# Kernel tuning notes

Measured on AMD Instinct MI355X. Metric: run time of the kernel, lower is better.

Reference implementation:

```python
import jax, jax.numpy as jnp
import numpy as np

D = 1024
H = 16
FFN = 4096
B = 4
S = 1024
EPS = 1e-12
NEG = -1e9


def _layernorm(x, gamma, beta):
    mean = x.mean(-1, keepdims=True)
    var = ((x - mean) ** 2).mean(-1, keepdims=True)  # biased var, matches unbiased=False
    return gamma * (x - mean) * jax.lax.rsqrt(var + EPS) + beta


def setup_inputs() -> dict:
    key = jax.random.key(0)
    ks = jax.random.split(key, 16)
    s_in = 1.0 / np.sqrt(D)
    s_ff = 1.0 / np.sqrt(FFN)
    return {
        "x": jax.random.normal(ks[0], (B, S, D), dtype=jnp.float32),
        "mask": jax.random.randint(ks[1], (B, H, S), 0, 2) > 0,  # bernoulli(0.5) key mask
        "Wqkv": jax.random.uniform(ks[2], (3 * D, D), minval=-s_in, maxval=s_in),
        "bqkv": jax.random.uniform(ks[3], (3 * D,), minval=-s_in, maxval=s_in),
        "Wo": jax.random.uniform(ks[4], (D, D), minval=-s_in, maxval=s_in),
        "bo": jax.random.uniform(ks[5], (D,), minval=-s_in, maxval=s_in),
        "W1": jax.random.uniform(ks[6], (FFN, D), minval=-s_in, maxval=s_in),
        "b1": jax.random.uniform(ks[7], (FFN,), minval=-s_in, maxval=s_in),
        "W2": jax.random.uniform(ks[8], (D, FFN), minval=-s_ff, maxval=s_ff),
        "b2": jax.random.uniform(ks[9], (D,), minval=-s_ff, maxval=s_ff),
        "g1": jnp.ones((D,), jnp.float32),
        "be1": jnp.zeros((D,), jnp.float32),
        "g2": jnp.ones((D,), jnp.float32),
        "be2": jnp.zeros((D,), jnp.float32),
    }


def reference(x, mask, Wqkv, bqkv, Wo, bo, W1, b1, W2, b2, g1, be1, g2, be2):
    b, s, _ = x.shape
    hd = D // H
    scale = hd ** -0.5

    # --- ProbSparseSelfAttention (dropout in eval mode) ---
    qkv = x @ Wqkv.T + bqkv                                   # [b, s, 3D]
    q, k, v = jnp.split(qkv, 3, axis=-1)
    q = q.reshape(b, s, H, hd).transpose(0, 2, 1, 3)          # [b, h, s, d]
    k = k.reshape(b, s, H, hd).transpose(0, 2, 1, 3)
    v = v.reshape(b, s, H, hd).transpose(0, 2, 1, 3)
    scores = jnp.einsum('bhid,bhjd->bhij', q * scale, k)      # [b, h, s, s]
    scores = jnp.where(mask[:, :, None, :], scores, NEG)      # mask keys (broadcast over i)
    attn = jax.nn.softmax(scores, axis=-1)
    ctx = jnp.einsum('bhij,bhjd->bhid', attn, v)
    ctx = ctx.transpose(0, 2, 1, 3).reshape(b, s, D)
    attn_out = ctx @ Wo.T + bo

    # residual + LayerNorm 1
    h = _layernorm(attn_out + x, g1, be1)

    # --- FFN ---
    ff = jax.nn.relu(h @ W1.T + b1) @ W2.T + b2

    # residual + LayerNorm 2
    return _layernorm(ff + h, g2, be2)
```

## Files before the change

kernel.cpp:

```cpp
#include <hip/hip_runtime.h>

#define DDIM 1024
#define FFN_DIM 4096
#define SS 1024
#define MTOK 4096

typedef __bf16 bf16x8 __attribute__((ext_vector_type(8)));
typedef float f32x4 __attribute__((ext_vector_type(4)));
typedef unsigned short ushort4v __attribute__((ext_vector_type(4)));
typedef unsigned short ushort8v __attribute__((ext_vector_type(8)));

__device__ __forceinline__ unsigned short f2bf(float f) {
    union { float f; unsigned u; } x;
    x.f = f;
    unsigned r = x.u + 0x7FFFu + ((x.u >> 16) & 1u);
    return (unsigned short)(r >> 16);
}
__device__ __forceinline__ float bf2f(unsigned short u) {
    union { unsigned u; float f; } x;
    x.u = (unsigned)u << 16;
    return x.f;
}

__device__ __forceinline__ int swz(int off) {
    return off ^ ((((off >> 7) & 7) ^ ((off >> 10) & 1)) << 4);
}
__device__ __forceinline__ int gswz(int b) {
    return b ^ (((b >> 7) & 7) << 4);
}

__device__ __forceinline__ void gload_lds16(const void* g, void* l) {
    __builtin_amdgcn_global_load_lds(
        (__attribute__((address_space(1))) unsigned int*)(unsigned long long)(g),
        (__attribute__((address_space(3))) unsigned int*)(l), 16, 0, 0);
}

__global__ __launch_bounds__(256) void cvt_bf16(const float* __restrict__ in,
                                                unsigned short* __restrict__ out, int n4) {
    int i = blockIdx.x * 256 + threadIdx.x;
    if (i < n4) {
        float4 v = ((const float4*)in)[i];
        ushort4v u = {f2bf(v.x), f2bf(v.y), f2bf(v.z), f2bf(v.w)};
        ((ushort4v*)out)[i] = u;
    }
}

template <int EPI, int SPLITK>
__global__ __launch_bounds__(512, 2) void gemm256(const unsigned short* __restrict__ A,
                                                  const unsigned short* __restrict__ B,
                                                  const float* __restrict__ bias,
                                                  unsigned short* __restrict__ O0,
                                                  unsigned short* __restrict__ O1,
                                                  unsigned short* __restrict__ O2,
                                                  unsigned short* __restrict__ O3,
                                                  int M, int N, int K) {
    __shared__ char smem[131072];
    const int tid = threadIdx.x;
    const int wid = tid >> 6, lane = tid & 63;
    const int wm = wid >> 2, wn = wid & 3;
    const int lr = lane & 15, lkb = (lane >> 4) * 16;
    const int m0 = blockIdx.y * 256, n0 = blockIdx.x * 256;
    const int z = blockIdx.z;
    const int Kc = K / SPLITK, kb = z * Kc;
    const int NT = Kc / 64;

    f32x4 acc[8][4];
#pragma unroll
    for (int i = 0; i < 8; i++)
#pragma unroll
        for (int j = 0; j < 4; j++) acc[i][j] = (f32x4){0.f, 0.f, 0.f, 0.f};

    auto stage_half = [&](int c, int t, int hs) {
        const int op = hs >> 1, h = hs & 1;
        const unsigned short* G = op ? B : A;
        const int r0 = (op ? n0 : m0) + h * 128;
        char* base = smem + c * 65536 + op * 32768 + h * 16384;
        const int k0 = kb + t * 64;
#pragma unroll
        for (int q = 0; q < 2; q++) {
            int d = q * 8192 + wid * 1024 + lane * 16;
            int s = gswz(d);
            int row = s >> 7, colb = s & 127;
            gload_lds16(G + (size_t)(r0 + row) * K + k0 + (colb >> 1),
                        base + q * 8192 + wid * 1024);
        }
    };

    stage_half(0, 0, 0); stage_half(0, 0, 1); stage_half(0, 0, 2); stage_half(0, 0, 3);
    asm volatile("s_waitcnt vmcnt(0)" ::: "memory");
    __syncthreads();

    for (int t = 0; t < NT; ++t) {
        const int c = t & 1;
        const char* Ab = smem + c * 65536;
        const char* Bb = Ab + 32768;
        const bool pre = (t + 1 < NT);
        bf16x8 bfr[4][2];
#pragma unroll
        for (int p = 0; p < 4; ++p) {
            bf16x8 afr[2][2];
#pragma unroll
            for (int mi = 0; mi < 2; mi++)
#pragma unroll
                for (int ks = 0; ks < 2; ks++) {
                    int b = (wm * 128 + (p * 2 + mi) * 16 + lr) * 128 + ks * 64 + lkb;
                    afr[mi][ks] = *(const bf16x8*)(Ab + gswz(b));
                }
            if (p == 0) {
#pragma unroll
                for (int nb = 0; nb < 4; nb++)
#pragma unroll
                    for (int ks = 0; ks < 2; ks++) {
                        int b = (wn * 64 + nb * 16 + lr) * 128 + ks * 64 + lkb;
                        bfr[nb][ks] = *(const bf16x8*)(Bb + gswz(b));
                    }
            }
            if (pre) stage_half(c ^ 1, t + 1, p);
            __builtin_amdgcn_s_barrier();
            asm volatile("s_waitcnt lgkmcnt(0)" ::: "memory");
            __builtin_amdgcn_sched_barrier(0);
            __builtin_amdgcn_s_setprio(1);
#pragma unroll
            for (int mi = 0; mi < 2; mi++)
#pragma unroll
                for (int nb = 0; nb < 4; nb++)
#pragma unroll
                    for (int ks = 0; ks < 2; ks++)
                        acc[p * 2 + mi][nb] = __builtin_amdgcn_mfma_f32_16x16x32_bf16(
                            afr[mi][ks], bfr[nb][ks], acc[p * 2 + mi][nb], 0, 0, 0);
            __builtin_amdgcn_s_setprio(0);
            if (p == 3 && pre) asm volatile("s_waitcnt vmcnt(0)" ::: "memory");
            __builtin_amdgcn_s_barrier();
        }
    }

    unsigned short* Op = (SPLITK == 1) ? O0 : (z == 0 ? O0 : z == 1 ? O1 : z == 2 ? O2 : O3);
    float bv[4];
#pragma unroll
    for (int nb = 0; nb < 4; nb++) bv[nb] = (z == 0) ? bias[n0 + wn * 64 + nb * 16 + lr] : 0.f;
    const int rr = (lane >> 4) * 4;
#pragma unroll
    for (int mb = 0; mb < 8; mb++)
#pragma unroll
        for (int nb = 0; nb < 4; nb++) {
            int col = n0 + wn * 64 + nb * 16 + lr;
#pragma unroll
            for (int r = 0; r < 4; r++) {
                int row = m0 + wm * 128 + mb * 16 + rr + r;
                float v = acc[mb][nb][r] + bv[nb];
                if (EPI == 2) v = fmaxf(v, 0.f);
                Op[(size_t)row * N + col] = f2bf(v);
            }
        }
}

__global__ __launch_bounds__(256) void gemm_bt(const unsigned short* __restrict__ A,
                                               const unsigned short* __restrict__ B,
                                               const float* __restrict__ bias,
                                               unsigned short* __restrict__ Cout,
                                               int M, int N, int K) {
    __shared__ unsigned short Asm[2][128 * 32];
    __shared__ unsigned short Bsm[2][128 * 32];
    const int tid = threadIdx.x;
    const int wid = tid >> 6, lane = tid & 63;
    const int m0 = blockIdx.y * 128, n0 = blockIdx.x * 128;
    const int lr = lane & 15, lk = (lane >> 4) * 8;
    const int wr = (wid >> 1) * 64, wc = (wid & 1) * 64;
    const int nkt = K / 32;

    f32x4 acc[4][4];
#pragma unroll
    for (int i = 0; i < 4; i++)
#pragma unroll
        for (int j = 0; j < 4; j++) acc[i][j] = (f32x4){0.f, 0.f, 0.f, 0.f};

    const unsigned short* Ag = A + (size_t)m0 * K;
    const unsigned short* Bg = B + (size_t)n0 * K;

    auto stage = [&](int buf, int k0) {
#pragma unroll
        for (int p = 0; p < 2; ++p) {
            int idx = p * 4096 + wid * 1024 + lane * 16;
            int row = idx >> 6, ce = (idx & 63) >> 1;
            gload_lds16(Ag + (size_t)row * K + k0 + ce, (char*)Asm[buf] + p * 4096 + wid * 1024);
            gload_lds16(Bg + (size_t)row * K + k0 + ce, (char*)Bsm[buf] + p * 4096 + wid * 1024);
        }
    };

    stage(0, 0);
    for (int kt = 0; kt < nkt; ++kt) {
        const int cur = kt & 1;
        __syncthreads();
        if (kt + 1 < nkt) stage(cur ^ 1, (kt + 1) * 32);
        bf16x8 af[4], bfr[4];
#pragma unroll
        for (int m = 0; m < 4; m++) af[m] = *(const bf16x8*)&Asm[cur][(wr + m * 16 + lr) * 32 + lk];
#pragma unroll
        for (int n = 0; n < 4; n++) bfr[n] = *(const bf16x8*)&Bsm[cur][(wc + n * 16 + lr) * 32 + lk];
#pragma unroll
        for (int m = 0; m < 4; m++)
#pragma unroll
            for (int n = 0; n < 4; n++)
                acc[m][n] = __builtin_amdgcn_mfma_f32_16x16x32_bf16(af[m], bfr[n], acc[m][n], 0, 0, 0);
    }

    float bv[4];
#pragma unroll
    for (int n = 0; n < 4; n++) bv[n] = bias[n0 + wc + n * 16 + lr];
    const int r0 = (lane >> 4) * 4;
#pragma unroll
    for (int m = 0; m < 4; m++)
#pragma unroll
        for (int n = 0; n < 4; n++) {
            int col = n0 + wc + n * 16 + lr;
#pragma unroll
            for (int r = 0; r < 4; r++) {
                int row = m0 + wr + m * 16 + r0 + r;
                Cout[(size_t)row * N + col] = f2bf(acc[m][n][r] + bv[n]);
            }
        }
}

__global__ __launch_bounds__(256) void vtrans(const unsigned short* __restrict__ qkv,
                                              unsigned short* __restrict__ vt) {
    __shared__ unsigned short T[64 * 64];
    const int tid = threadIdx.x;
    const int bh = blockIdx.y, b = bh >> 4, h = bh & 15;
    const int s0 = blockIdx.x * 64;
    const unsigned short* src = qkv + (size_t)(b * SS + s0) * 3072 + 2048 + h * 64;
#pragma unroll
    for (int p = 0; p < 2; p++) {
        int idx = p * 4096 + tid * 16;
        int row = idx >> 7, ce = (idx & 127) >> 1;
        ushort8v v = *(const ushort8v*)(src + (size_t)row * 3072 + ce);
        *(ushort8v*)((char*)T + swz(idx)) = v;
    }
    __syncthreads();
    unsigned short* dst = vt + (size_t)bh * 64 * SS + s0;
#pragma unroll
    for (int p = 0; p < 2; p++) {
        int idx = p * 4096 + tid * 16;
        int d = idx >> 7, t0 = (idx & 127) >> 1;
        ushort8v o;
#pragma unroll
        for (int i = 0; i < 8; i++)
            o[i] = *(const unsigned short*)((char*)T + swz((t0 + i) * 128 + d * 2));
        *(ushort8v*)(dst + (size_t)d * SS + t0) = o;
    }
}

__global__ __launch_bounds__(256) void attn_fused(const unsigned short* __restrict__ qkv,
                                                  const unsigned short* __restrict__ vt,
                                                  const int* __restrict__ mask,
                                                  unsigned short* __restrict__ ctx) {
    __shared__ unsigned short Ksm[2][64 * 64];
    __shared__ unsigned short Vsm[2][64 * 64];
    __shared__ unsigned short Psm[4][16 * 64];
    __shared__ float maskadd[2][64];
    const int tid = threadIdx.x, wid = tid >> 6, lane = tid & 63;
    const int bid = blockIdx.x;
    const int xcd = bid & 7, loc = bid >> 3;
    const int bh = xcd * 8 + (loc >> 4), q0 = (loc & 15) * 64;
    const int b = bh >> 4, h = bh & 15;
    const int lr = lane & 15, lk2 = (lane >> 4) * 16;
    const size_t base = (size_t)b * SS * 3072 + h * 64;
    const float SC2 = 0.18033688011112042f;

    bf16x8 qf[2];
    {
        const unsigned short* qp = qkv + base + (size_t)(q0 + wid * 16 + lr) * 3072;
        qf[0] = *(const bf16x8*)(qp + (lk2 >> 1));
        qf[1] = *(const bf16x8*)(qp + 32 + (lk2 >> 1));
    }
    float m_run[4] = {-3e38f, -3e38f, -3e38f, -3e38f};
    float l_run[4] = {0.f, 0.f, 0.f, 0.f};
    f32x4 oacc[4];
#pragma unroll
    for (int i = 0; i < 4; i++) oacc[i] = (f32x4){0.f, 0.f, 0.f, 0.f};

    const unsigned short* Kgb = qkv + base + 1024;
    const unsigned short* Vgb = vt + (size_t)bh * 64 * SS;

    auto stage = [&](int buf, int kt) {
#pragma unroll
        for (int p = 0; p < 2; p++) {
            int idx = p * 4096 + wid * 1024 + lane * 16;
            int s = swz(idx);
            int row = s >> 7, ce = (s & 127) >> 1;
            gload_lds16(Kgb + (size_t)(kt * 64 + row) * 3072 + ce,
                        (char*)Ksm[buf] + p * 4096 + wid * 1024);
            gload_lds16(Vgb + (size_t)row * SS + kt * 64 + ce,
                        (char*)Vsm[buf] + p * 4096 + wid * 1024);
        }
        if (tid < 64) maskadd[buf][tid] = mask[bh * SS + kt * 64 + tid] ? 0.f : -1.5e9f;
    };

    stage(0, 0);
    for (int kt = 0; kt < SS / 64; ++kt) {
        const int cur = kt & 1;
        __syncthreads();
        if (kt < SS / 64 - 1) stage(cur ^ 1, kt + 1);
        const char* Kb = (const char*)Ksm[cur];
        const char* Vb = (const char*)Vsm[cur];

        f32x4 sc[4];
#pragma unroll
        for (int nt = 0; nt < 4; nt++) {
            f32x4 a = (f32x4){0.f, 0.f, 0.f, 0.f};
            int rowb = (nt * 16 + lr) * 128;
            bf16x8 k0v = *(const bf16x8*)(Kb + swz(rowb + lk2));
            bf16x8 k1v = *(const bf16x8*)(Kb + swz(rowb + 64 + lk2));
            a = __builtin_amdgcn_mfma_f32_16x16x32_bf16(qf[0], k0v, a, 0, 0, 0);
            a = __builtin_amdgcn_mfma_f32_16x16x32_bf16(qf[1], k1v, a, 0, 0, 0);
            sc[nt] = a;
        }
        float mk[4];
#pragma unroll
        for (int nt = 0; nt < 4; nt++) mk[nt] = maskadd[cur][nt * 16 + lr];
        float pmax[4];
#pragma unroll
        for (int r = 0; r < 4; r++) {
            float v = -3e38f;
#pragma unroll
            for (int nt = 0; nt < 4; nt++) {
                float s = sc[nt][r] * SC2 + mk[nt];
                sc[nt][r] = s;
                v = fmaxf(v, s);
            }
            v = fmaxf(v, __shfl_xor(v, 1));
            v = fmaxf(v, __shfl_xor(v, 2));
            v = fmaxf(v, __shfl_xor(v, 4));
            v = fmaxf(v, __shfl_xor(v, 8));
            pmax[r] = v;
        }
        bool okt = true;
#pragma unroll
        for (int r = 0; r < 4; r++) okt = okt && (pmax[r] <= m_run[r] + 8.f);
        const bool skip = __all(okt);
        if (!skip) {
#pragma unroll
            for (int r = 0; r < 4; r++) {
                float mnew = fmaxf(m_run[r], pmax[r]);
                float alpha = exp2f(m_run[r] - mnew);
                m_run[r] = mnew;
                l_run[r] *= alpha;
#pragma unroll
                for (int dt = 0; dt < 4; dt++) oacc[dt][r] *= alpha;
            }
        }
#pragma unroll
        for (int r = 0; r < 4; r++) {
            float ls = 0.f;
#pragma unroll
            for (int nt = 0; nt < 4; nt++) {
                float pexp = exp2f(sc[nt][r] - m_run[r]);
                sc[nt][r] = pexp;
                ls += pexp;
            }
            ls += __shfl_xor(ls, 1);
            ls += __shfl_xor(ls, 2);
            ls += __shfl_xor(ls, 4);
            ls += __shfl_xor(ls, 8);
            l_run[r] += ls;
        }
        const int prow = (lane >> 4) * 4;
        char* Pb = (char*)Psm[wid];
#pragma unroll
        for (int nt = 0; nt < 4; nt++)
#pragma unroll
            for (int r = 0; r < 4; r++)
                *(unsigned short*)(Pb + swz((prow + r) * 128 + (nt * 16 + lr) * 2)) = f2bf(sc[nt][r]);
        bf16x8 pf0 = *(const bf16x8*)(Pb + swz(lr * 128 + lk2));
        bf16x8 pf1 = *(const bf16x8*)(Pb + swz(lr * 128 + 64 + lk2));
#pragma unroll
        for (int dt = 0; dt < 4; dt++) {
            int rowb = (dt * 16 + lr) * 128;
            bf16x8 v0 = *(const bf16x8*)(Vb + swz(rowb + lk2));
            bf16x8 v1 = *(const bf16x8*)(Vb + swz(rowb + 64 + lk2));
            oacc[dt] = __builtin_amdgcn_mfma_f32_16x16x32_bf16(pf0, v0, oacc[dt], 0, 0, 0);
            oacc[dt] = __builtin_amdgcn_mfma_f32_16x16x32_bf16(pf1, v1, oacc[dt], 0, 0, 0);
        }
    }
#pragma unroll
    for (int dt = 0; dt < 4; dt++)
#pragma unroll
        for (int r = 0; r < 4; r++) {
            float v = oacc[dt][r] / l_run[r];
            int row = q0 + wid * 16 + (lane >> 4) * 4 + r;
            ctx[(size_t)(b * SS + row) * DDIM + h * 64 + dt * 16 + lr] = f2bf(v);
        }
}

__global__ __launch_bounds__(256) void resid_ln1(const unsigned short* __restrict__ attno,
                                                 const float* __restrict__ x,
                                                 const float* __restrict__ gamma,
                                                 const float* __restrict__ beta,
                                                 unsigned short* __restrict__ hbf) {
    __shared__ float red[16];
    const int row = blockIdx.x, tid = threadIdx.x;
    const int wid = tid >> 6, lane = tid & 63;
    ushort4v av = ((const ushort4v*)(attno + (size_t)row * DDIM))[tid];
    float4 bv = ((const float4*)(x + (size_t)row * DDIM))[tid];
    float4 v;
    v.x = bf2f(av[0]) + bv.x; v.y = bf2f(av[1]) + bv.y;
    v.z = bf2f(av[2]) + bv.z; v.w = bf2f(av[3]) + bv.w;
    float s = v.x + v.y + v.z + v.w;
    float s2 = v.x * v.x + v.y * v.y + v.z * v.z + v.w * v.w;
#pragma unroll
    for (int off = 1; off < 64; off <<= 1) { s += __shfl_xor(s, off); s2 += __shfl_xor(s2, off); }
    if (lane == 0) { red[wid] = s; red[8 + wid] = s2; }
    __syncthreads();
    s = red[0] + red[1] + red[2] + red[3];
    s2 = red[8] + red[9] + red[10] + red[11];
    float mean = s * (1.f / 1024.f);
    float var = s2 * (1.f / 1024.f) - mean * mean;
    float rstd = rsqrtf(var + 1e-12f);
    float4 g = ((const float4*)gamma)[tid];
    float4 be = ((const float4*)beta)[tid];
    ushort4v u = {f2bf(g.x * (v.x - mean) * rstd + be.x),
                  f2bf(g.y * (v.y - mean) * rstd + be.y),
                  f2bf(g.z * (v.z - mean) * rstd + be.z),
                  f2bf(g.w * (v.w - mean) * rstd + be.w)};
    ((ushort4v*)(hbf + (size_t)row * DDIM))[tid] = u;
}

__global__ __launch_bounds__(256) void resid_ln2(const unsigned short* __restrict__ p0,
                                                 const unsigned short* __restrict__ p1,
                                                 const unsigned short* __restrict__ p2,
                                                 const unsigned short* __restrict__ p3,
                                                 const unsigned short* __restrict__ hbf,
                                                 const float* __restrict__ gamma,
                                                 const float* __restrict__ beta,
                                                 float* __restrict__ out) {
    __shared__ float red[16];
    const int row = blockIdx.x, tid = threadIdx.x;
    const int wid = tid >> 6, lane = tid & 63;
    size_t off = (size_t)row * DDIM;
    ushort4v a0 = ((const ushort4v*)(p0 + off))[tid];
    ushort4v a1 = ((const ushort4v*)(p1 + off))[tid];
    ushort4v a2 = ((const ushort4v*)(p2 + off))[tid];
    ushort4v a3 = ((const ushort4v*)(p3 + off))[tid];
    ushort4v hv = ((const ushort4v*)(hbf + off))[tid];
    float4 v;
    v.x = bf2f(a0[0]) + bf2f(a1[0]) + bf2f(a2[0]) + bf2f(a3[0]) + bf2f(hv[0]);
    v.y = bf2f(a0[1]) + bf2f(a1[1]) + bf2f(a2[1]) + bf2f(a3[1]) + bf2f(hv[1]);
    v.z = bf2f(a0[2]) + bf2f(a1[2]) + bf2f(a2[2]) + bf2f(a3[2]) + bf2f(hv[2]);
    v.w = bf2f(a0[3]) + bf2f(a1[3]) + bf2f(a2[3]) + bf2f(a3[3]) + bf2f(hv[3]);
    float s = v.x + v.y + v.z + v.w;
    float s2 = v.x * v.x + v.y * v.y + v.z * v.z + v.w * v.w;
#pragma unroll
    for (int off2 = 1; off2 < 64; off2 <<= 1) { s += __shfl_xor(s, off2); s2 += __shfl_xor(s2, off2); }
    if (lane == 0) { red[wid] = s; red[8 + wid] = s2; }
    __syncthreads();
    s = red[0] + red[1] + red[2] + red[3];
    s2 = red[8] + red[9] + red[10] + red[11];
    float mean = s * (1.f / 1024.f);
    float var = s2 * (1.f / 1024.f) - mean * mean;
    float rstd = rsqrtf(var + 1e-12f);
    float4 g = ((const float4*)gamma)[tid];
    float4 be = ((const float4*)beta)[tid];
    float4 o;
    o.x = g.x * (v.x - mean) * rstd + be.x;
    o.y = g.y * (v.y - mean) * rstd + be.y;
    o.z = g.z * (v.z - mean) * rstd + be.z;
    o.w = g.w * (v.w - mean) * rstd + be.w;
    ((float4*)(out + off))[tid] = o;
}

extern "C" void kernel_launch(void* const* d_in, const int* in_sizes, int n_in,
                              void* d_out, int out_size, void* d_ws, size_t ws_size,
                              hipStream_t stream) {
    const float* x    = (const float*)d_in[0];
    const int*   mask = (const int*)d_in[1];
    const float* Wqkv = (const float*)d_in[2];
    const float* bqkv = (const float*)d_in[3];
    const float* Wo   = (const float*)d_in[4];
    const float* bo   = (const float*)d_in[5];
    const float* W1   = (const float*)d_in[6];
    const float* b1   = (const float*)d_in[7];
    const float* W2   = (const float*)d_in[8];
    const float* b2   = (const float*)d_in[9];
    const float* g1   = (const float*)d_in[10];
    const float* be1  = (const float*)d_in[11];
    const float* g2   = (const float*)d_in[12];
    const float* be2  = (const float*)d_in[13];
    float* out = (float*)d_out;

    char* ws = (char*)d_ws;
    unsigned short* xbf   = (unsigned short*)(ws + 0);
    unsigned short* vtb   = (unsigned short*)(ws + 0);
    unsigned short* p0    = (unsigned short*)(ws + 0);
    unsigned short* qkvbf = (unsigned short*)(ws + (8ull << 20));
    unsigned short* ff1   = (unsigned short*)(ws + (8ull << 20));
    unsigned short* ctx   = (unsigned short*)(ws + (32ull << 20));
    unsigned short* w1b   = (unsigned short*)(ws + (40ull << 20));
    unsigned short* p1    = (unsigned short*)(ws + (40ull << 20));
    unsigned short* w2b   = (unsigned short*)(ws + (48ull << 20));
    unsigned short* wqkvb = (unsigned short*)(ws + (56ull << 20));
    unsigned short* p2    = (unsigned short*)(ws + (56ull << 20));
    unsigned short* wob   = (unsigned short*)(ws + (62ull << 20));
    unsigned short* attno = (unsigned short*)(ws + (64ull << 20));
    unsigned short* p3    = (unsigned short*)(ws + (64ull << 20));
    unsigned short* hbf   = (unsigned short*)(ws + (72ull << 20));

    cvt_bf16<<<4096, 256, 0, stream>>>(x, xbf, 1048576);
    cvt_bf16<<<3072, 256, 0, stream>>>(Wqkv, wqkvb, 786432);
    cvt_bf16<<<1024, 256, 0, stream>>>(Wo, wob, 262144);
    cvt_bf16<<<4096, 256, 0, stream>>>(W1, w1b, 1048576);
    cvt_bf16<<<4096, 256, 0, stream>>>(W2, w2b, 1048576);

    gemm256<1, 1><<<dim3(12, 16, 1), 512, 0, stream>>>(xbf, wqkvb, bqkv,
        qkvbf, qkvbf, qkvbf, qkvbf, MTOK, 3072, 1024);
    vtrans<<<dim3(16, 64), 256, 0, stream>>>(qkvbf, vtb);
    attn_fused<<<1024, 256, 0, stream>>>(qkvbf, vtb, mask, ctx);
    gemm_bt<<<dim3(8, 32), 256, 0, stream>>>(ctx, wob, bo, attno, MTOK, 1024, 1024);
    resid_ln1<<<4096, 256, 0, stream>>>(attno, x, g1, be1, hbf);
    gemm256<2, 1><<<dim3(16, 16, 1), 512, 0, stream>>>(hbf, w1b, b1,
        ff1, ff1, ff1, ff1, MTOK, FFN_DIM, 1024);
    gemm256<1, 4><<<dim3(4, 16, 4), 512, 0, stream>>>(ff1, w2b, b2,
        p0, p1, p2, p3, MTOK, DDIM, FFN_DIM);
    resid_ln2<<<4096, 256, 0, stream>>>(p0, p1, p2, p3, hbf, g2, be2, out);
}
```

Measured before the change: 372.2 us.

## Merge fp32-to-bf16 conversions into one launch and issue full-tile prefetch at once

The five separate conversion kernels are replaced by a single kernel that picks source and destination by thread index, which removes four launches and their tail gaps. In the 256x256 GEMM, the next K-tile's global-to-LDS loads are now all issued in the first sub-step instead of being spread over four sub-steps. The float-to-bf16 helper now uses the compiler's native cast instead of manual rounding. Issuing all prefetch loads at once may raise VMEM pressure early and shift how well loads overlap with MFMA work.

```diff
diff --git a/kernel.cpp b/kernel.cpp
--- a/kernel.cpp
+++ b/kernel.cpp
@@ -11,10 +11,8 @@
 typedef unsigned short ushort8v __attribute__((ext_vector_type(8)));
 
 __device__ __forceinline__ unsigned short f2bf(float f) {
-    union { float f; unsigned u; } x;
-    x.f = f;
-    unsigned r = x.u + 0x7FFFu + ((x.u >> 16) & 1u);
-    return (unsigned short)(r >> 16);
+    __bf16 h = (__bf16)f;
+    return __builtin_bit_cast(unsigned short, h);
 }
 __device__ __forceinline__ float bf2f(unsigned short u) {
     union { unsigned u; float f; } x;
@@ -35,14 +33,28 @@
         (__attribute__((address_space(3))) unsigned int*)(l), 16, 0, 0);
 }
 
-__global__ __launch_bounds__(256) void cvt_bf16(const float* __restrict__ in,
-                                                unsigned short* __restrict__ out, int n4) {
+__global__ __launch_bounds__(256) void cvt_all(const float* __restrict__ x,
+                                               const float* __restrict__ wqkv,
+                                               const float* __restrict__ wo,
+                                               const float* __restrict__ w1,
+                                               const float* __restrict__ w2,
+                                               unsigned short* __restrict__ xbf,
+                                               unsigned short* __restrict__ wqkvb,
+                                               unsigned short* __restrict__ wob,
+                                               unsigned short* __restrict__ w1b,
+                                               unsigned short* __restrict__ w2b) {
     int i = blockIdx.x * 256 + threadIdx.x;
-    if (i < n4) {
-        float4 v = ((const float4*)in)[i];
-        ushort4v u = {f2bf(v.x), f2bf(v.y), f2bf(v.z), f2bf(v.w)};
-        ((ushort4v*)out)[i] = u;
-    }
+    const float* src;
+    unsigned short* dst;
+    int off;
+    if (i < 1048576)      { src = x;    dst = xbf;   off = i; }
+    else if (i < 1835008) { src = wqkv; dst = wqkvb; off = i - 1048576; }
+    else if (i < 2097152) { src = wo;   dst = wob;   off = i - 1835008; }
+    else if (i < 3145728) { src = w1;   dst = w1b;   off = i - 2097152; }
+    else                  { src = w2;   dst = w2b;   off = i - 3145728; }
+    float4 v = ((const float4*)src)[off];
+    ushort4v u = {f2bf(v.x), f2bf(v.y), f2bf(v.z), f2bf(v.w)};
+    ((ushort4v*)dst)[off] = u;
 }
 
 template <int EPI, int SPLITK>
@@ -70,23 +82,25 @@
 #pragma unroll
         for (int j = 0; j < 4; j++) acc[i][j] = (f32x4){0.f, 0.f, 0.f, 0.f};
 
-    auto stage_half = [&](int c, int t, int hs) {
-        const int op = hs >> 1, h = hs & 1;
-        const unsigned short* G = op ? B : A;
-        const int r0 = (op ? n0 : m0) + h * 128;
-        char* base = smem + c * 65536 + op * 32768 + h * 16384;
+    auto stage_tile = [&](int c, int t) {
         const int k0 = kb + t * 64;
 #pragma unroll
-        for (int q = 0; q < 2; q++) {
-            int d = q * 8192 + wid * 1024 + lane * 16;
-            int s = gswz(d);
-            int row = s >> 7, colb = s & 127;
-            gload_lds16(G + (size_t)(r0 + row) * K + k0 + (colb >> 1),
-                        base + q * 8192 + wid * 1024);
+        for (int hs = 0; hs < 4; ++hs) {
+            const int op = hs >> 1, h = hs & 1;
+            const unsigned short* G = op ? B : A;
+            const int r0 = (op ? n0 : m0) + h * 128;
+            char* base = smem + c * 65536 + op * 32768 + h * 16384;
+#pragma unroll
+            for (int q = 0; q < 2; q++) {
+                int d = q * 8192 + wid * 1024 + lane * 16;
+                int s = gswz(d);
+                gload_lds16(G + (size_t)(r0 + (s >> 7)) * K + k0 + ((s & 127) >> 1),
+                            base + q * 8192 + wid * 1024);
+            }
         }
     };
 
-    stage_half(0, 0, 0); stage_half(0, 0, 1); stage_half(0, 0, 2); stage_half(0, 0, 3);
+    stage_tile(0, 0);
     asm volatile("s_waitcnt vmcnt(0)" ::: "memory");
     __syncthreads();
 
@@ -114,8 +128,8 @@
                         int b = (wn * 64 + nb * 16 + lr) * 128 + ks * 64 + lkb;
                         bfr[nb][ks] = *(const bf16x8*)(Bb + gswz(b));
                     }
-            }
-            if (pre) stage_half(c ^ 1, t + 1, p);
+                if (pre) stage_tile(c ^ 1, t + 1);
+            }
             __builtin_amdgcn_s_barrier();
             asm volatile("s_waitcnt lgkmcnt(0)" ::: "memory");
             __builtin_amdgcn_sched_barrier(0);
@@ -503,11 +517,7 @@
     unsigned short* p3    = (unsigned short*)(ws + (64ull << 20));
     unsigned short* hbf   = (unsigned short*)(ws + (72ull << 20));
 
-    cvt_bf16<<<4096, 256, 0, stream>>>(x, xbf, 1048576);
-    cvt_bf16<<<3072, 256, 0, stream>>>(Wqkv, wqkvb, 786432);
-    cvt_bf16<<<1024, 256, 0, stream>>>(Wo, wob, 262144);
-    cvt_bf16<<<4096, 256, 0, stream>>>(W1, w1b, 1048576);
-    cvt_bf16<<<4096, 256, 0, stream>>>(W2, w2b, 1048576);
+    cvt_all<<<16384, 256, 0, stream>>>(x, Wqkv, Wo, W1, W2, xbf, wqkvb, wob, w1b, w2b);
 
     gemm256<1, 1><<<dim3(12, 16, 1), 512, 0, stream>>>(xbf, wqkvb, bqkv,
         qkvbf, qkvbf, qkvbf, qkvbf, MTOK, 3072, 1024);
```

Result: faster. 356.1 us (-4.3%).
